# Kernel optimization log

Measured on AMD Instinct MI355X. Metric: run time of the kernel, lower is better.

## Reference

```python
import jax, jax.numpy as jnp
import numpy as np

B, N, J, P = 64, 2048, 32, 64   # instances, ops per instance, jobs, ops per job (N = J*P)
D, H = 128, 128                 # out_size_ope, hidden_size_ope
NEG_SLOPE = 0.2


def _kaiming(key, fan_in, fan_out):
    return jax.random.normal(key, (fan_in, fan_out), jnp.float32) * np.sqrt(2.0 / fan_in)


def _mlp(x, W1, b1, W2, b2):
    # nn.Sequential(Linear, ELU, Linear)
    return jax.nn.elu(x @ W1 + b1) @ W2 + b2


def setup_inputs() -> dict:
    key = jax.random.key(0)
    ks = jax.random.split(key, 4)
    features = jax.random.normal(ks[0], (B, N, D), jnp.float32)
    job_starts = jnp.arange(J, dtype=jnp.int32) * P                      # first op of each job block
    offsets = jax.random.randint(ks[1], (B, J), 0, P)                    # current position within block
    ope_step_batch = job_starts[None, :] + offsets                       # [B, J], step_j in [start_j, end_j]
    end_ope_biases_batch = jnp.broadcast_to(job_starts + (P - 1), (B, J))
    opes_appertain_batch = jnp.broadcast_to(jnp.repeat(jnp.arange(J, dtype=jnp.int32), P)[None, :], (B, N))
    batch_idxes = jnp.arange(B, dtype=jnp.int32)
    inp = {
        'features': features,
        'discount_r': jnp.float32(0.9),
        'ope_step_batch': ope_step_batch,
        'end_ope_biases_batch': end_ope_biases_batch,
        'opes_appertain_batch': opes_appertain_batch,
        'batch_idxes': batch_idxes,
    }
    for i, nm in enumerate(['fw', 'zj', 'pr']):
        k1, k2 = jax.random.split(jax.random.fold_in(ks[2], i))
        inp[nm + '_W1'] = _kaiming(k1, D, H)
        inp[nm + '_b1'] = jnp.zeros((H,), jnp.float32)
        inp[nm + '_W2'] = _kaiming(k2, H, D)
        inp[nm + '_b2'] = jnp.zeros((D,), jnp.float32)
    return inp


def reference(features, discount_r,
              fw_W1, fw_b1, fw_W2, fw_b2,
              zj_W1, zj_b1, zj_W2, zj_b2,
              pr_W1, pr_b1, pr_W2, pr_b2,
              ope_step_batch, end_ope_biases_batch, opes_appertain_batch, batch_idxes):
    # opes_appertain_batch is accepted but unused, exactly like the torch forward.
    f32 = features.dtype
    steps = ope_step_batch[batch_idxes]        # [B, J]
    ends = end_ope_biases_batch[batch_idxes]   # [B, J]
    i = jnp.arange(N)

    # --- per-job descending update loop, vectorized ---
    # op i is updated iff step_j < i <= end_j for its job j; descending order in the
    # original means feat[i-1] is still the ORIGINAL value, so updates are independent.
    memb = (i[None, None, :] > steps[:, :, None]) & (i[None, None, :] <= ends[:, :, None])  # [B,J,N]
    updated = jnp.any(memb, axis=1)                                                         # [B,N]
    step_of = jnp.sum(jnp.where(memb, steps[:, :, None], 0), axis=1)                        # [B,N]
    rpow = discount_r ** (i[None, :] - step_of).astype(f32)                                 # r^(i - step)
    feat_prev = jnp.concatenate([jnp.zeros_like(features[:, :1]), features[:, :-1]], axis=1)
    # aggregate(MEAN): agg_f_w(feat_pre) + agg_f_w(feat_sub * r)
    cand = _mlp(features, fw_W1, fw_b1, fw_W2, fw_b2) + \
           _mlp(feat_prev * rpow[..., None], fw_W1, fw_b1, fw_W2, fw_b2)
    feat1 = jnp.where(updated[..., None], cand, features)

    # --- collect feat at each valid job's current step (step positions are never updated) ---
    collected = jax.vmap(lambda f, s: f[s])(features, steps)   # [B, J, D]
    valid = steps <= ends                                      # [B, J]
    n = jnp.sum(valid, axis=1).astype(f32)                     # [B]
    S = jnp.sum(jnp.where(valid[..., None], collected, 0.0), axis=1)  # [B, D]
    # aggregate_dif: new[j] = agg_z_j((old[j] + r * sum_{k!=j} old[k]) / n)
    mixed = (collected + discount_r * (S[:, None, :] - collected)) / n[:, None, None]
    z = _mlp(mixed, zj_W1, zj_b1, zj_W2, zj_b2)                # [B, J, D]

    # faithful replication of feat_opt[b][save_index[k]] = features_all[k]
    # (writes at op positions equal to JOB indices 0..J-1, for valid jobs)
    head = jnp.where(valid[..., None], z, feat1[:, :J, :])
    feat2 = feat1.at[:, :J, :].set(head)

    out = jax.nn.leaky_relu(_mlp(feat2, pr_W1, pr_b1, pr_W2, pr_b2), NEG_SLOPE)
    return out
```

## Files before the change

kernel.cpp:

```cpp
#include <hip/hip_runtime.h>

#define B_ 64
#define N_ 2048
#define J_ 32
#define D_ 128
#define NEG_SLOPE_ 0.2f

typedef __attribute__((ext_vector_type(4))) float f32x4;
typedef __attribute__((ext_vector_type(8))) __bf16 bf16x8;
typedef __attribute__((ext_vector_type(4))) __bf16 bf16x4;

#define ACT_NONE 0
#define ACT_ELU 1
#define ACT_LEAKY 2

template<int ACT>
__device__ __forceinline__ float apply_act(float v) {
    if constexpr (ACT == ACT_ELU)        return v > 0.f ? v : __expf(v) - 1.f;
    else if constexpr (ACT == ACT_LEAKY) return v >= 0.f ? v : NEG_SLOPE_ * v;
    else return v;
}

__device__ __forceinline__ bf16x8 frag_ld(const __bf16* src, int row, int kc) {
    return *(const bf16x8*)&src[row * D_ + ((kc ^ (row & 7)) << 3)];
}

__device__ __forceinline__ void load_wregs1(const __bf16* __restrict__ wmat,
                                            int wst, int ln, int lq, bf16x8 wr_[4]) {
#pragma unroll
    for (int ks = 0; ks < 4; ++ks)
        wr_[ks] = frag_ld(wmat, wst * 16 + ln, ks * 4 + lq);
}

__device__ __forceinline__ void st_row(__bf16* dst, int row, int ch,
                                       float4 f0, float4 f1, float s) {
    bf16x8 u;
    u[0] = (__bf16)(f0.x * s); u[1] = (__bf16)(f0.y * s);
    u[2] = (__bf16)(f0.z * s); u[3] = (__bf16)(f0.w * s);
    u[4] = (__bf16)(f1.x * s); u[5] = (__bf16)(f1.y * s);
    u[6] = (__bf16)(f1.z * s); u[7] = (__bf16)(f1.w * s);
    *(bf16x8*)&dst[row * D_ + ((ch ^ (row & 7)) << 3)] = u;
}

__device__ __forceinline__ void gemmS64(const __bf16* xb, const bf16x8 wr_[4],
                                        int ln, int lq, f32x4 acc[4]) {
    const f32x4 z = {0.f, 0.f, 0.f, 0.f};
#pragma unroll
    for (int nt = 0; nt < 4; ++nt) acc[nt] = z;
#pragma unroll
    for (int ks = 0; ks < 4; ++ks) {
        const int kc = ks * 4 + lq;
#pragma unroll
        for (int nt = 0; nt < 4; ++nt) {
            const bf16x8 b = frag_ld(xb, nt * 16 + ln, kc);
            acc[nt] = __builtin_amdgcn_mfma_f32_16x16x32_bf16(wr_[ks], b, acc[nt], 0, 0, 0);
        }
    }
}

template<bool INIT>
__device__ __forceinline__ void gemmS32(const __bf16* xb, const bf16x8 wr_[4],
                                        int ln, int lq, f32x4 acc[2]) {
    if constexpr (INIT) {
        const f32x4 z = {0.f, 0.f, 0.f, 0.f};
        acc[0] = z; acc[1] = z;
    }
#pragma unroll
    for (int ks = 0; ks < 4; ++ks) {
        const int kc = ks * 4 + lq;
        const bf16x8 b0 = frag_ld(xb, ln, kc);
        const bf16x8 b1 = frag_ld(xb, 16 + ln, kc);
        acc[0] = __builtin_amdgcn_mfma_f32_16x16x32_bf16(wr_[ks], b0, acc[0], 0, 0, 0);
        acc[1] = __builtin_amdgcn_mfma_f32_16x16x32_bf16(wr_[ks], b1, acc[1], 0, 0, 0);
    }
}

template<int ACT>
__device__ __forceinline__ void epiS64_lds(const f32x4 acc[4], __bf16* dst,
                                           const float* __restrict__ bias,
                                           int wst, int ln, int lq) {
    const int cb = wst * 16 + lq * 4;
    const f32x4 bv = *(const f32x4*)&bias[cb];
#pragma unroll
    for (int nt = 0; nt < 4; ++nt) {
        const int jr = nt * 16 + ln;
        bf16x4 o;
#pragma unroll
        for (int r = 0; r < 4; ++r)
            o[r] = (__bf16)apply_act<ACT>(acc[nt][r] + bv[r]);
        *(bf16x4*)&dst[jr * D_ + (((cb >> 3) ^ (jr & 7)) << 3) + (cb & 7)] = o;
    }
}

template<int ACT>
__device__ __forceinline__ void epiS32_lds(const f32x4 acc[2], __bf16* dst, int rowoff,
                                           const float* __restrict__ bias,
                                           int wst, int ln, int lq) {
    const int cb = wst * 16 + lq * 4;
    const f32x4 bv = *(const f32x4*)&bias[cb];
#pragma unroll
    for (int nt = 0; nt < 2; ++nt) {
        const int jr = rowoff + nt * 16 + ln;
        bf16x4 o;
#pragma unroll
        for (int r = 0; r < 4; ++r)
            o[r] = (__bf16)apply_act<ACT>(acc[nt][r] + bv[r]);
        *(bf16x4*)&dst[jr * D_ + (((cb >> 3) ^ (jr & 7)) << 3) + (cb & 7)] = o;
    }
}

__global__ __launch_bounds__(256) void k_prep(
    const float* __restrict__ w0, const float* __restrict__ w1,
    const float* __restrict__ w2, const float* __restrict__ w3,
    const float* __restrict__ w4, const float* __restrict__ w5,
    __bf16* __restrict__ wdst,
    const float* __restrict__ F, const int* __restrict__ STEP,
    const int* __restrict__ ENDB, const int* __restrict__ BIDX,
    float* __restrict__ Sbuf, int* __restrict__ nvalid) {
    const int t = threadIdx.x;
    if (blockIdx.x < 6) {
        const float* src;
        switch (blockIdx.x) {
            case 0: src = w0; break; case 1: src = w1; break; case 2: src = w2; break;
            case 3: src = w3; break; case 4: src = w4; break; default: src = w5; break;
        }
        __bf16* d = wdst + (size_t)blockIdx.x * D_ * D_;
        for (int id = t; id < D_ * 16; id += 256) {
            const int n = id >> 4, ch = id & 15;
            bf16x8 u;
#pragma unroll
            for (int j = 0; j < 8; ++j) u[j] = (__bf16)src[(ch * 8 + j) * D_ + n];
            *(bf16x8*)&d[n * D_ + ((ch ^ (n & 7)) << 3)] = u;
        }
        return;
    }
    const int b = blockIdx.x - 6;
    __shared__ int steps_s[J_];
    __shared__ int valid_s[J_];
    __shared__ int nv;
    const int bi = BIDX[b];
    if (t == 0) nv = 0;
    __syncthreads();
    if (t < J_) {
        const int s = STEP[bi * J_ + t];
        const int e = ENDB[bi * J_ + t];
        steps_s[t] = s;
        const int v = (s <= e) ? 1 : 0;
        valid_s[t] = v;
        if (v) atomicAdd(&nv, 1);
    }
    __syncthreads();
    if (t < D_) {
        float acc = 0.f;
        for (int j = 0; j < J_; ++j)
            if (valid_s[j]) acc += F[((size_t)b * N_ + steps_s[j]) * D_ + t];
        Sbuf[b * D_ + t] = acc;
    }
    if (t == 0) nvalid[b] = nv;
}

__global__ __launch_bounds__(512, 4) void k_fused(
    const float* __restrict__ F, const float* __restrict__ rp_,
    const __bf16* __restrict__ wsW,
    const float* __restrict__ fb1, const float* __restrict__ fb2,
    const float* __restrict__ zb1, const float* __restrict__ zb2,
    const float* __restrict__ pb1, const float* __restrict__ pb2,
    const int* __restrict__ STEP, const int* __restrict__ ENDB,
    const int* __restrict__ BIDX, const float* __restrict__ Sbuf,
    const int* __restrict__ nvalid, float* __restrict__ out) {
    __shared__ __bf16 xs[64 * D_];
    __shared__ __bf16 hs[64 * D_];

    const int t = threadIdx.x;
    const int lane = t & 63, wst = t >> 6;
    const int ln = lane & 15, lq = lane >> 4;
    const int bid = (blockIdx.x & 7) * 512 + (blockIdx.x >> 3);
    const int b = bid >> 6, ti = bid & 63;
    const int r0 = ti * 32;
    const int bi = BIDX[b];
    const int jb = ti >> 1;
    const int s_j = STEP[bi * J_ + jb];
    const int e_j = ENDB[bi * J_ + jb];
    const float r = *rp_;
    const float l2r = __log2f(r);
    const int lo = (s_j + 1 > r0) ? s_j + 1 : r0;
    const int hi = (e_j < r0 + 31) ? e_j : r0 + 31;
    const bool has_upd = lo <= hi;
    const bool head_tile = (ti == 0);

    const float* Fb = F + (size_t)b * N_ * D_;
    const int rr_ = t >> 4;
    const int ch_ = t & 15;
    const int rA = r0 + rr_;
    const float* qA = Fb + (size_t)rA * D_ + ch_ * 8;
    const float4 xa0 = *(const float4*)qA, xa1 = *(const float4*)(qA + 4);
    float4 ya0, ya1;
    float scA = 0.f;
    if (has_upd) {
        const bool uA = (rA > s_j) && (rA <= e_j);
        scA = uA ? exp2f((float)(rA - s_j) * l2r) : 0.f;
        const float* uqA = Fb + (size_t)(uA ? rA - 1 : rA) * D_ + ch_ * 8;
        ya0 = *(const float4*)uqA; ya1 = *(const float4*)(uqA + 4);
    }
    bf16x8 wA[4];
    load_wregs1(has_upd ? wsW : wsW + 2 * 16384, wst, ln, lq, wA);

    st_row(xs, rr_, ch_, xa0, xa1, 1.f);
    if (has_upd) st_row(xs, rr_ + 32, ch_, ya0, ya1, scA);
    __syncthreads();

    if (has_upd) {
        f32x4 acc[4];
        gemmS64(xs, wA, ln, lq, acc);
        bf16x8 wB[4];
        load_wregs1(wsW + 16384, wst, ln, lq, wB);
        epiS64_lds<ACT_ELU>(acc, hs, fb1, wst, ln, lq);
        __syncthreads();
        f32x4 a2[2];
        gemmS32<true>(hs, wB, ln, lq, a2);
        gemmS32<false>(hs + 32 * D_, wB, ln, lq, a2);
        const int cb = wst * 16 + lq * 4;
        const f32x4 bv = *(const f32x4*)&fb2[cb];
#pragma unroll
        for (int nt = 0; nt < 2; ++nt) {
            const int row = nt * 16 + ln;
            const int i = r0 + row;
            if (!((i > s_j) && (i <= e_j))) continue;
            bf16x4 o;
#pragma unroll
            for (int rr2 = 0; rr2 < 4; ++rr2)
                o[rr2] = (__bf16)(a2[nt][rr2] + 2.f * bv[rr2]);
            *(bf16x4*)&xs[row * D_ + (((cb >> 3) ^ (row & 7)) << 3) + (cb & 7)] = o;
        }
    }

    if (head_tile) {
        __syncthreads();
        const float n_ = (float)nvalid[b];
        const float inv = (n_ > 0.f) ? 1.f / n_ : 0.f;
        {
            const int row = t >> 4, ch = t & 15;
            const int sr = STEP[bi * J_ + row];
            const float* cr = Fb + (size_t)sr * D_ + ch * 8;
            const float4 c0 = *(const float4*)cr, c1 = *(const float4*)(cr + 4);
            const float4 s0 = *(const float4*)(Sbuf + b * D_ + ch * 8);
            const float4 s1 = *(const float4*)(Sbuf + b * D_ + ch * 8 + 4);
            bf16x8 u;
            u[0] = (__bf16)((c0.x + r * (s0.x - c0.x)) * inv);
            u[1] = (__bf16)((c0.y + r * (s0.y - c0.y)) * inv);
            u[2] = (__bf16)((c0.z + r * (s0.z - c0.z)) * inv);
            u[3] = (__bf16)((c0.w + r * (s0.w - c0.w)) * inv);
            u[4] = (__bf16)((c1.x + r * (s1.x - c1.x)) * inv);
            u[5] = (__bf16)((c1.y + r * (s1.y - c1.y)) * inv);
            u[6] = (__bf16)((c1.z + r * (s1.z - c1.z)) * inv);
            u[7] = (__bf16)((c1.w + r * (s1.w - c1.w)) * inv);
            *(bf16x8*)&hs[row * D_ + ((ch ^ (row & 7)) << 3)] = u;
        }
        __syncthreads();
        {
            bf16x8 wza[4];
            load_wregs1(wsW + 4 * 16384, wst, ln, lq, wza);
            f32x4 az[2];
            gemmS32<true>(hs, wza, ln, lq, az);
            epiS32_lds<ACT_ELU>(az, hs, 32, zb1, wst, ln, lq);
        }
        __syncthreads();
        {
            bf16x8 wzb[4];
            load_wregs1(wsW + 5 * 16384, wst, ln, lq, wzb);
            f32x4 az[2];
            gemmS32<true>(hs + 32 * D_, wzb, ln, lq, az);
            const int cb = wst * 16 + lq * 4;
            const f32x4 bv = *(const f32x4*)&zb2[cb];
#pragma unroll
            for (int nt = 0; nt < 2; ++nt) {
                const int row = nt * 16 + ln;
                const int sr = STEP[bi * J_ + row];
                const int er = ENDB[bi * J_ + row];
                if (sr > er) continue;
                bf16x4 o;
#pragma unroll
                for (int rr2 = 0; rr2 < 4; ++rr2)
                    o[rr2] = (__bf16)(az[nt][rr2] + bv[rr2]);
                *(bf16x4*)&xs[row * D_ + (((cb >> 3) ^ (row & 7)) << 3) + (cb & 7)] = o;
            }
        }
    }

    if (has_upd || head_tile) {
        load_wregs1(wsW + 2 * 16384, wst, ln, lq, wA);
        __syncthreads();
    }

    f32x4 ap[2];
    gemmS32<true>(xs, wA, ln, lq, ap);
    bf16x8 wB2[4];
    load_wregs1(wsW + 3 * 16384, wst, ln, lq, wB2);
    epiS32_lds<ACT_ELU>(ap, hs, 0, pb1, wst, ln, lq);
    __syncthreads();

    gemmS32<true>(hs, wB2, ln, lq, ap);
    float* outb = out + ((size_t)b * N_ + r0) * D_;
    const int cb = wst * 16 + lq * 4;
    const f32x4 bv = *(const f32x4*)&pb2[cb];
#pragma unroll
    for (int nt = 0; nt < 2; ++nt) {
        const int jr = nt * 16 + ln;
        f32x4 o;
#pragma unroll
        for (int rr2 = 0; rr2 < 4; ++rr2)
            o[rr2] = apply_act<ACT_LEAKY>(ap[nt][rr2] + bv[rr2]);
        *(f32x4*)&outb[(size_t)jr * D_ + cb] = o;
    }
}

extern "C" void kernel_launch(void* const* d_in, const int* in_sizes, int n_in,
                              void* d_out, int out_size, void* d_ws, size_t ws_size,
                              hipStream_t stream) {
    const float* F    = (const float*)d_in[0];
    const float* rp   = (const float*)d_in[1];
    const int*  STEP  = (const int*)d_in[2];
    const int*  ENDB  = (const int*)d_in[3];
    const int*  BIDX  = (const int*)d_in[5];
    const float* fwW1 = (const float*)d_in[6];
    const float* fwb1 = (const float*)d_in[7];
    const float* fwW2 = (const float*)d_in[8];
    const float* fwb2 = (const float*)d_in[9];
    const float* zjW1 = (const float*)d_in[10];
    const float* zjb1 = (const float*)d_in[11];
    const float* zjW2 = (const float*)d_in[12];
    const float* zjb2 = (const float*)d_in[13];
    const float* prW1 = (const float*)d_in[14];
    const float* prb1 = (const float*)d_in[15];
    const float* prW2 = (const float*)d_in[16];
    const float* prb2 = (const float*)d_in[17];
    float* out = (float*)d_out;

    char* ws = (char*)d_ws;
    __bf16* wsW = (__bf16*)ws;
    float* Sbuf = (float*)(ws + 393216);
    int* nvalid = (int*)(ws + 425984);

    hipLaunchKernelGGL(k_prep, dim3(70), dim3(256), 0, stream,
                       fwW1, fwW2, prW1, prW2, zjW1, zjW2, wsW,
                       F, STEP, ENDB, BIDX, Sbuf, nvalid);
    hipLaunchKernelGGL(k_fused, dim3(B_ * 64), dim3(512), 0, stream,
                       F, rp, wsW, fwb1, fwb2, zjb1, zjb2, prb1, prb2,
                       STEP, ENDB, BIDX, Sbuf, nvalid, out);
}
```

Before: 61.52 us.

## Process both 32-row tiles of a job per block with prefetch of second tile

```diff
diff --git a/kernel.cpp b/kernel.cpp
--- a/kernel.cpp
+++ b/kernel.cpp
@@ -109,105 +109,18 @@
     }
 }
 
-__global__ __launch_bounds__(256) void k_prep(
-    const float* __restrict__ w0, const float* __restrict__ w1,
-    const float* __restrict__ w2, const float* __restrict__ w3,
-    const float* __restrict__ w4, const float* __restrict__ w5,
-    __bf16* __restrict__ wdst,
-    const float* __restrict__ F, const int* __restrict__ STEP,
-    const int* __restrict__ ENDB, const int* __restrict__ BIDX,
-    float* __restrict__ Sbuf, int* __restrict__ nvalid) {
-    const int t = threadIdx.x;
-    if (blockIdx.x < 6) {
-        const float* src;
-        switch (blockIdx.x) {
-            case 0: src = w0; break; case 1: src = w1; break; case 2: src = w2; break;
-            case 3: src = w3; break; case 4: src = w4; break; default: src = w5; break;
-        }
-        __bf16* d = wdst + (size_t)blockIdx.x * D_ * D_;
-        for (int id = t; id < D_ * 16; id += 256) {
-            const int n = id >> 4, ch = id & 15;
-            bf16x8 u;
-#pragma unroll
-            for (int j = 0; j < 8; ++j) u[j] = (__bf16)src[(ch * 8 + j) * D_ + n];
-            *(bf16x8*)&d[n * D_ + ((ch ^ (n & 7)) << 3)] = u;
-        }
-        return;
-    }
-    const int b = blockIdx.x - 6;
-    __shared__ int steps_s[J_];
-    __shared__ int valid_s[J_];
-    __shared__ int nv;
-    const int bi = BIDX[b];
-    if (t == 0) nv = 0;
-    __syncthreads();
-    if (t < J_) {
-        const int s = STEP[bi * J_ + t];
-        const int e = ENDB[bi * J_ + t];
-        steps_s[t] = s;
-        const int v = (s <= e) ? 1 : 0;
-        valid_s[t] = v;
-        if (v) atomicAdd(&nv, 1);
-    }
-    __syncthreads();
-    if (t < D_) {
-        float acc = 0.f;
-        for (int j = 0; j < J_; ++j)
-            if (valid_s[j]) acc += F[((size_t)b * N_ + steps_s[j]) * D_ + t];
-        Sbuf[b * D_ + t] = acc;
-    }
-    if (t == 0) nvalid[b] = nv;
-}
-
-__global__ __launch_bounds__(512, 4) void k_fused(
-    const float* __restrict__ F, const float* __restrict__ rp_,
-    const __bf16* __restrict__ wsW,
+__device__ __forceinline__ void tile_compute(
+    __bf16* xs, __bf16* hs, const __bf16* __restrict__ wsW,
     const float* __restrict__ fb1, const float* __restrict__ fb2,
     const float* __restrict__ zb1, const float* __restrict__ zb2,
     const float* __restrict__ pb1, const float* __restrict__ pb2,
-    const int* __restrict__ STEP, const int* __restrict__ ENDB,
-    const int* __restrict__ BIDX, const float* __restrict__ Sbuf,
-    const int* __restrict__ nvalid, float* __restrict__ out) {
-    __shared__ __bf16 xs[64 * D_];
-    __shared__ __bf16 hs[64 * D_];
-
-    const int t = threadIdx.x;
-    const int lane = t & 63, wst = t >> 6;
-    const int ln = lane & 15, lq = lane >> 4;
-    const int bid = (blockIdx.x & 7) * 512 + (blockIdx.x >> 3);
-    const int b = bid >> 6, ti = bid & 63;
-    const int r0 = ti * 32;
-    const int bi = BIDX[b];
-    const int jb = ti >> 1;
-    const int s_j = STEP[bi * J_ + jb];
-    const int e_j = ENDB[bi * J_ + jb];
-    const float r = *rp_;
-    const float l2r = __log2f(r);
-    const int lo = (s_j + 1 > r0) ? s_j + 1 : r0;
-    const int hi = (e_j < r0 + 31) ? e_j : r0 + 31;
-    const bool has_upd = lo <= hi;
-    const bool head_tile = (ti == 0);
-
-    const float* Fb = F + (size_t)b * N_ * D_;
-    const int rr_ = t >> 4;
-    const int ch_ = t & 15;
-    const int rA = r0 + rr_;
-    const float* qA = Fb + (size_t)rA * D_ + ch_ * 8;
-    const float4 xa0 = *(const float4*)qA, xa1 = *(const float4*)(qA + 4);
-    float4 ya0, ya1;
-    float scA = 0.f;
-    if (has_upd) {
-        const bool uA = (rA > s_j) && (rA <= e_j);
-        scA = uA ? exp2f((float)(rA - s_j) * l2r) : 0.f;
-        const float* uqA = Fb + (size_t)(uA ? rA - 1 : rA) * D_ + ch_ * 8;
-        ya0 = *(const float4*)uqA; ya1 = *(const float4*)(uqA + 4);
-    }
+    const int* __restrict__ STEP, const int* __restrict__ ENDB, int bi,
+    const float* __restrict__ Sbuf, const int* __restrict__ nvalid,
+    const float* __restrict__ Fb, float* __restrict__ out, int b,
+    int r0, int s_j, int e_j, bool has_upd, bool head_tile,
+    float r, float l2r, int wst, int ln, int lq, int t) {
     bf16x8 wA[4];
     load_wregs1(has_upd ? wsW : wsW + 2 * 16384, wst, ln, lq, wA);
-
-    st_row(xs, rr_, ch_, xa0, xa1, 1.f);
-    if (has_upd) st_row(xs, rr_ + 32, ch_, ya0, ya1, scA);
-    __syncthreads();
 
     if (has_upd) {
         f32x4 acc[4];
@@ -312,6 +225,133 @@
             o[rr2] = apply_act<ACT_LEAKY>(ap[nt][rr2] + bv[rr2]);
         *(f32x4*)&outb[(size_t)jr * D_ + cb] = o;
     }
+}
+
+__global__ __launch_bounds__(256) void k_prep(
+    const float* __restrict__ w0, const float* __restrict__ w1,
+    const float* __restrict__ w2, const float* __restrict__ w3,
+    const float* __restrict__ w4, const float* __restrict__ w5,
+    __bf16* __restrict__ wdst,
+    const float* __restrict__ F, const int* __restrict__ STEP,
+    const int* __restrict__ ENDB, const int* __restrict__ BIDX,
+    float* __restrict__ Sbuf, int* __restrict__ nvalid) {
+    const int t = threadIdx.x;
+    if (blockIdx.x < 6) {
+        const float* src;
+        switch (blockIdx.x) {
+            case 0: src = w0; break; case 1: src = w1; break; case 2: src = w2; break;
+            case 3: src = w3; break; case 4: src = w4; break; default: src = w5; break;
+        }
+        __bf16* d = wdst + (size_t)blockIdx.x * D_ * D_;
+        for (int id = t; id < D_ * 16; id += 256) {
+            const int n = id >> 4, ch = id & 15;
+            bf16x8 u;
+#pragma unroll
+            for (int j = 0; j < 8; ++j) u[j] = (__bf16)src[(ch * 8 + j) * D_ + n];
+            *(bf16x8*)&d[n * D_ + ((ch ^ (n & 7)) << 3)] = u;
+        }
+        return;
+    }
+    const int b = blockIdx.x - 6;
+    __shared__ int steps_s[J_];
+    __shared__ int valid_s[J_];
+    __shared__ int nv;
+    const int bi = BIDX[b];
+    if (t == 0) nv = 0;
+    __syncthreads();
+    if (t < J_) {
+        const int s = STEP[bi * J_ + t];
+        const int e = ENDB[bi * J_ + t];
+        steps_s[t] = s;
+        const int v = (s <= e) ? 1 : 0;
+        valid_s[t] = v;
+        if (v) atomicAdd(&nv, 1);
+    }
+    __syncthreads();
+    if (t < D_) {
+        float acc = 0.f;
+        for (int j = 0; j < J_; ++j)
+            if (valid_s[j]) acc += F[((size_t)b * N_ + steps_s[j]) * D_ + t];
+        Sbuf[b * D_ + t] = acc;
+    }
+    if (t == 0) nvalid[b] = nv;
+}
+
+__global__ __launch_bounds__(512, 4) void k_fused(
+    const float* __restrict__ F, const float* __restrict__ rp_,
+    const __bf16* __restrict__ wsW,
+    const float* __restrict__ fb1, const float* __restrict__ fb2,
+    const float* __restrict__ zb1, const float* __restrict__ zb2,
+    const float* __restrict__ pb1, const float* __restrict__ pb2,
+    const int* __restrict__ STEP, const int* __restrict__ ENDB,
+    const int* __restrict__ BIDX, const float* __restrict__ Sbuf,
+    const int* __restrict__ nvalid, float* __restrict__ out) {
+    __shared__ __bf16 xs[64 * D_];
+    __shared__ __bf16 hs[64 * D_];
+
+    const int t = threadIdx.x;
+    const int lane = t & 63, wst = t >> 6;
+    const int ln = lane & 15, lq = lane >> 4;
+    const int bid = (blockIdx.x & 7) * 256 + (blockIdx.x >> 3);
+    const int b = bid >> 5, q = bid & 31;
+    const int r0A = q * 64, r0B = r0A + 32;
+    const int bi = BIDX[b];
+    const int s_j = STEP[bi * J_ + q];
+    const int e_j = ENDB[bi * J_ + q];
+    const float r = *rp_;
+    const float l2r = __log2f(r);
+    const int loA = (s_j + 1 > r0A) ? s_j + 1 : r0A;
+    const int hiA = (e_j < r0A + 31) ? e_j : r0A + 31;
+    const bool updA = loA <= hiA;
+    const int loB = (s_j + 1 > r0B) ? s_j + 1 : r0B;
+    const int hiB = (e_j < r0B + 31) ? e_j : r0B + 31;
+    const bool updB = loB <= hiB;
+    const bool headA = (q == 0);
+
+    const float* Fb = F + (size_t)b * N_ * D_;
+    const int rr_ = t >> 4;
+    const int ch_ = t & 15;
+
+    {
+        const int rA = r0A + rr_;
+        const float* qA = Fb + (size_t)rA * D_ + ch_ * 8;
+        const float4 xa0 = *(const float4*)qA, xa1 = *(const float4*)(qA + 4);
+        float4 ya0, ya1;
+        float scA = 0.f;
+        if (updA) {
+            const bool uA = (rA > s_j) && (rA <= e_j);
+            scA = uA ? exp2f((float)(rA - s_j) * l2r) : 0.f;
+            const float* uqA = Fb + (size_t)(uA ? rA - 1 : rA) * D_ + ch_ * 8;
+            ya0 = *(const float4*)uqA; ya1 = *(const float4*)(uqA + 4);
+        }
+        st_row(xs, rr_, ch_, xa0, xa1, 1.f);
+        if (updA) st_row(xs, rr_ + 32, ch_, ya0, ya1, scA);
+    }
+
+    const int rB = r0B + rr_;
+    const float* qB = Fb + (size_t)rB * D_ + ch_ * 8;
+    const float4 xb0 = *(const float4*)qB, xb1 = *(const float4*)(qB + 4);
+    float4 yb0, yb1;
+    float scB = 0.f;
+    if (updB) {
+        const bool uB = (rB > s_j) && (rB <= e_j);
+        scB = uB ? exp2f((float)(rB - s_j) * l2r) : 0.f;
+        const float* uqB = Fb + (size_t)(uB ? rB - 1 : rB) * D_ + ch_ * 8;
+        yb0 = *(const float4*)uqB; yb1 = *(const float4*)(uqB + 4);
+    }
+    __syncthreads();
+
+    tile_compute(xs, hs, wsW, fb1, fb2, zb1, zb2, pb1, pb2,
+                 STEP, ENDB, bi, Sbuf, nvalid, Fb, out, b,
+                 r0A, s_j, e_j, updA, headA, r, l2r, wst, ln, lq, t);
+
+    st_row(xs, rr_, ch_, xb0, xb1, 1.f);
+    if (updB) st_row(xs, rr_ + 32, ch_, yb0, yb1, scB);
+    __syncthreads();
+
+    tile_compute(xs, hs, wsW, fb1, fb2, zb1, zb2, pb1, pb2,
+                 STEP, ENDB, bi, Sbuf, nvalid, Fb, out, b,
+                 r0B, s_j, e_j, updB, false, r, l2r, wst, ln, lq, t);
 }
 
 extern "C" void kernel_launch(void* const* d_in, const int* in_sizes, int n_in,
@@ -344,7 +384,7 @@
     hipLaunchKernelGGL(k_prep, dim3(70), dim3(256), 0, stream,
                        fwW1, fwW2, prW1, prW2, zjW1, zjW2, wsW,
                        F, STEP, ENDB, BIDX, Sbuf, nvalid);
-    hipLaunchKernelGGL(k_fused, dim3(B_ * 64), dim3(512), 0, stream,
+    hipLaunchKernelGGL(k_fused, dim3(B_ * 32), dim3(512), 0, stream,
                        F, rp, wsW, fwb1, fwb2, zjb1, zjb2, prb1, prb2,
                        STEP, ENDB, BIDX, Sbuf, nvalid, out);
 }
```

Measured after the change: 65.56 us. 1.07x slower.
